# Kernel optimization log

Measured on AMD Instinct MI355X. Metric: run time of the kernel, lower is better.

The kernel has to match this reference:

```python
import jax, jax.numpy as jnp
import numpy as np

N, F, DEG, C = 20000, 64, 16, 16   # nodes, features, in-degree incl. self loop, classes
E = N * (DEG - 1)                   # regular (non-self-loop) edges


def setup_inputs() -> dict:
    key = jax.random.key(0)
    ks = jax.random.split(key, 12)
    x = jax.random.normal(ks[0], (N, F), dtype=jnp.float32)
    src = jax.random.randint(ks[1], (E,), 0, N, dtype=jnp.int32)
    dst = jnp.repeat(jnp.arange(N, dtype=jnp.int32), DEG - 1)  # exactly DEG-1 in-edges/node
    edge_index = jnp.stack([src, dst])
    s = 1.0 / np.sqrt(F)
    params = {}
    for i, kw, kb in ((1, ks[2], ks[3]), (2, ks[4], ks[5]), (3, ks[6], ks[7])):
        params[f"W{i}"] = jax.random.normal(kw, (F, F), dtype=jnp.float32) * s
        params[f"b{i}"] = jax.random.normal(kb, (F,), dtype=jnp.float32) * s
    params["Wfc"] = jax.random.normal(ks[8], (C, F), dtype=jnp.float32) * s
    params["bfc"] = jax.random.normal(ks[9], (C,), dtype=jnp.float32) * s
    return {"x": x, "edge_index": edge_index, **params}


def _pca_conv(h, src, dst, W, b):
    # GCNConv.forward: linear first, then propagate with symmetric normalization.
    hl = h @ W.T                                             # [N, F]
    # add self loops (appended after regular edges, as in PyG)
    loop = jnp.arange(N, dtype=src.dtype)
    src_a = jnp.concatenate([src, loop])
    dst_a = jnp.concatenate([dst, loop])
    deg = jnp.zeros((N,), hl.dtype).at[dst_a].add(1.0)
    dinv = jax.lax.rsqrt(deg)
    norm = dinv[src_a] * dinv[dst_a]                         # [Ea]
    m = norm[:, None] * hl[src_a]                            # messages [Ea, F]
    # aggregate(): pack each destination's messages contiguously, in edge order
    order = jnp.argsort(dst_a)                               # stable sort by destination
    sd = dst_a[order]
    slot = jnp.arange(sd.shape[0]) - jnp.searchsorted(sd, sd, side='left')
    neigh = jnp.zeros((N, DEG, F), hl.dtype).at[sd, slot].set(m[order])
    neigh = neigh.reshape(N, DEG * F)                        # [N, max_degree*F]
    # torch.pca_lowrank(neigh, q=F, center=True): top-F right singular vectors of
    # the column-centered matrix; computed via eigh on the (DEG*F x DEG*F) Gram.
    Xc = neigh - jnp.mean(neigh, axis=0, keepdims=True)
    G = Xc.T @ Xc                                            # [DEG*F, DEG*F]
    _, V = jnp.linalg.eigh(G)                                # ascending eigenvalues
    Vtop = V[:, ::-1][:, :F]                                 # top-F principal directions
    proj = neigh @ Vtop                                      # note: projects UNcentered neigh
    return proj @ W.T + b                                    # self.lin again + bias


def reference(x, edge_index, W1, b1, W2, b2, W3, b3, Wfc, bfc):
    src, dst = edge_index[0], edge_index[1]
    h = jax.nn.relu(_pca_conv(x, src, dst, W1, b1))
    h = jax.nn.relu(_pca_conv(h, src, dst, W2, b2))
    h = jax.nn.relu(_pca_conv(h, src, dst, W3, b3))
    out = h @ Wfc.T + bfc
    return jax.nn.log_softmax(out, axis=-1)
```

## Files before the change

kernel.cpp:

```cpp
#include <hip/hip_runtime.h>
#include <cmath>

#define NNODES 20000
#define FD 64
#define EPN 15
#define NB 1024
#define BSUB 80
#define NCLS 16
#define NPAIR 40

__global__ __launch_bounds__(256) void k_linT(const float* __restrict__ X,
    const float* __restrict__ W, const float* __restrict__ bias,
    float* __restrict__ out, int ncol, int relu)
{
  __shared__ float Wsh[64][65];
  __shared__ float Xsh[64][65];
  int t = threadIdx.x;
  int r0 = blockIdx.x * 64;
  for (int idx = t; idx < ncol * 64; idx += 256) Wsh[idx >> 6][idx & 63] = W[idx];
  for (int idx = t; idx < 64 * 64; idx += 256) {
    int r = idx >> 6, c = idx & 63;
    Xsh[r][c] = (r0 + r < NNODES) ? X[(size_t)(r0 + r) * 64 + c] : 0.f;
  }
  __syncthreads();
  for (int idx = t; idx < 64 * ncol; idx += 256) {
    int r = idx / ncol, o = idx % ncol;
    float acc = 0.f;
    #pragma unroll
    for (int j = 0; j < 64; j++) acc += Xsh[r][j] * Wsh[o][j];
    if (bias) acc += bias[o];
    if (relu) acc = fmaxf(acc, 0.f);
    if (r0 + r < NNODES) out[(size_t)(r0 + r) * ncol + o] = acc;
  }
}

__global__ __launch_bounds__(256) void k_meanslot(const float* __restrict__ hl,
    const int* __restrict__ src, float* __restrict__ mus)
{
  int k = blockIdx.x;
  int part = blockIdx.y;
  int t = threadIdx.x;
  int c = t & 63, sub = t >> 6;
  int d0 = part * 2500;
  float acc = 0.f;
  for (int d = d0 + sub; d < d0 + 2500; d += 4) {
    int row = (k < EPN) ? src[d * EPN + k] : d;
    acc += hl[(size_t)row * 64 + c];
  }
  __shared__ float red[4][64];
  red[sub][c] = acc;
  __syncthreads();
  if (t < 64) {
    float s = red[0][t] + red[1][t] + red[2][t] + red[3][t];
    atomicAdd(&mus[k * 64 + t], s * (1.f / 20000.f));
  }
}

__global__ __launch_bounds__(256) void k_buildX(const float* __restrict__ hl,
    const int* __restrict__ src, const float* __restrict__ mus,
    float* __restrict__ X)
{
  __shared__ float4 mu4[256];
  int t = threadIdx.x;
  int d0 = blockIdx.x * 64;
  mu4[t] = ((const float4*)mus)[t];
  __syncthreads();
  for (int k = 0; k < 16; k++) {
    for (int item = t; item < 1024; item += 256) {
      int rr = item >> 4, f4 = item & 15;
      int d = d0 + rr;
      if (d < NNODES) {
        int row = (k < EPN) ? src[d * EPN + k] : d;
        float4 v = ((const float4*)hl)[(size_t)row * 16 + f4];
        float4 m = mu4[k * 16 + f4];
        v.x -= m.x; v.y -= m.y; v.z -= m.z; v.w -= m.w;
        ((float4*)X)[(size_t)d * 256 + k * 16 + f4] = v;
      }
    }
  }
}

__global__ __launch_bounds__(256) void k_syrkX(const float* __restrict__ X,
    float* __restrict__ TP, int rows)
{
  __shared__ float As[32][128];
  __shared__ float Bs[32][128];
  int t = threadIdx.x;
  int pr = blockIdx.x, I = 0, rem = pr;
  for (int ii = 0; ii < 8; ii++) {
    int cnt = 8 - ii;
    if (rem < cnt) { I = ii; break; }
    rem -= cnt;
  }
  int J = I + rem;
  int d0 = blockIdx.y * rows;
  int d1 = d0 + rows;
  int a0 = (t & 15) * 4, b0 = (t >> 4) * 4;
  float acc[8][8] = {};
  for (int dc = d0; dc < d1; dc += 32) {
    __syncthreads();
    for (int item = t; item < 1024; item += 256) {
      int rr = item >> 5, c4 = item & 31;
      int d = dc + rr;
      float4 va = make_float4(0.f, 0.f, 0.f, 0.f), vb = va;
      if (d < d1) {
        va = ((const float4*)X)[(size_t)d * 256 + I * 32 + c4];
        vb = ((const float4*)X)[(size_t)d * 256 + J * 32 + c4];
      }
      *(float4*)&As[rr][c4 * 4] = va;
      *(float4*)&Bs[rr][c4 * 4] = vb;
    }
    __syncthreads();
    for (int dd = 0; dd < 32; dd++) {
      float av[8], bv[8];
      *(float4*)&av[0] = *(const float4*)&As[dd][a0];
      *(float4*)&av[4] = *(const float4*)&As[dd][a0 + 64];
      *(float4*)&bv[0] = *(const float4*)&Bs[dd][b0];
      *(float4*)&bv[4] = *(const float4*)&Bs[dd][b0 + 64];
      #pragma unroll
      for (int x = 0; x < 8; x++)
        #pragma unroll
        for (int y = 0; y < 8; y++) acc[x][y] += av[x] * bv[y];
    }
  }
  float* Tout = TP + (size_t)blockIdx.y * ((size_t)NB * NB);
  #pragma unroll
  for (int x = 0; x < 8; x++) {
    int rowi = I * 128 + ((x < 4) ? (a0 + x) : (64 + a0 + x - 4));
    size_t base = (size_t)rowi * NB + J * 128;
    *(float4*)&Tout[base + b0]      = make_float4(acc[x][0], acc[x][1], acc[x][2], acc[x][3]);
    *(float4*)&Tout[base + 64 + b0] = make_float4(acc[x][4], acc[x][5], acc[x][6], acc[x][7]);
  }
}

__global__ __launch_bounds__(256) void k_assembleG16(const float* __restrict__ TP,
    float* __restrict__ G, int ns)
{
  size_t idx = (size_t)blockIdx.x * 256 + threadIdx.x;
  int p = (int)(idx >> 10), q = (int)(idx & 1023);
  int ti = p >> 6, tj = q >> 6;
  size_t e = (ti <= tj) ? idx : (((size_t)q << 10) | (size_t)p);
  float v = 0.f;
  for (int s2 = 0; s2 < ns; s2++) v += TP[(size_t)s2 * ((size_t)NB * NB) + e];
  G[idx] = v * (1.f / 256.f);
}

__global__ __launch_bounds__(256) void k_gram(const float* __restrict__ hl,
    const int* __restrict__ src, const float* __restrict__ mus,
    float* __restrict__ T)
{
  __shared__ float Ash[64][64];
  __shared__ float Bsh[64][64];
  __shared__ float muA[64], muB[64];
  int t = threadIdx.x;
  int pr = blockIdx.x, i = 0, rem = pr;
  for (int ii = 0; ii < 16; ii++) {
    int cnt = 16 - ii;
    if (rem < cnt) { i = ii; break; }
    rem -= cnt;
  }
  int j = i + rem;
  if (t < 64) muA[t] = mus[i * 64 + t];
  else if (t < 128) muB[t - 64] = mus[j * 64 + (t - 64)];
  float acc[4][4] = {};
  int a0 = (t & 15) * 4, b0 = (t >> 4) * 4;
  int d0 = blockIdx.y * 4000, d1 = d0 + 4000;
  for (int dc = d0; dc < d1; dc += 64) {
    __syncthreads();
    for (int item = t; item < 1024; item += 256) {
      int rr = item >> 4, f4 = item & 15;
      int d = dc + rr;
      float4 va = make_float4(0.f, 0.f, 0.f, 0.f);
      float4 vb = va;
      if (d < d1) {
        int ra = (i < EPN) ? src[d * EPN + i] : d;
        int rb = (j < EPN) ? src[d * EPN + j] : d;
        va = ((const float4*)hl)[(size_t)ra * 16 + f4];
        vb = ((const float4*)hl)[(size_t)rb * 16 + f4];
        int cb = f4 * 4;
        va.x -= muA[cb]; va.y -= muA[cb + 1]; va.z -= muA[cb + 2]; va.w -= muA[cb + 3];
        vb.x -= muB[cb]; vb.y -= muB[cb + 1]; vb.z -= muB[cb + 2]; vb.w -= muB[cb + 3];
      }
      ((float4*)&Ash[rr][0])[f4] = va;
      ((float4*)&Bsh[rr][0])[f4] = vb;
    }
    __syncthreads();
    for (int dd = 0; dd < 64; dd++) {
      float av[4], bv[4];
      #pragma unroll
      for (int u = 0; u < 4; u++) av[u] = Ash[dd][a0 + u];
      #pragma unroll
      for (int u = 0; u < 4; u++) bv[u] = Bsh[dd][b0 + u];
      #pragma unroll
      for (int x = 0; x < 4; x++)
        #pragma unroll
        for (int y = 0; y < 4; y++) acc[x][y] += av[x] * bv[y];
    }
  }
  #pragma unroll
  for (int x = 0; x < 4; x++)
    #pragma unroll
    for (int y = 0; y < 4; y++)
      atomicAdd(&T[(size_t)(i * 64 + a0 + x) * NB + (j * 64 + b0 + y)], acc[x][y]);
}

__global__ __launch_bounds__(256) void k_assembleG(const float* __restrict__ T,
    float* __restrict__ G)
{
  size_t idx = (size_t)blockIdx.x * 256 + threadIdx.x;
  int p = (int)(idx >> 10), q = (int)(idx & 1023);
  int ti = p >> 6, tj = q >> 6;
  float v = (ti <= tj) ? T[idx] : T[((size_t)q << 10) | (size_t)p];
  G[idx] = v * (1.f / 256.f);
}

__global__ __launch_bounds__(256) void k_gemmG2(const float* __restrict__ G,
    float* __restrict__ G2)
{
  __shared__ float Ash[64][68];
  __shared__ float Bsh[64][68];
  int t = threadIdx.x;
  int bi = blockIdx.x * 64, bj = blockIdx.y * 64;
  int a0 = (t & 15) * 4, b0 = (t >> 4) * 4;
  float acc[4][4] = {};
  for (int d0 = 0; d0 < NB; d0 += 64) {
    __syncthreads();
    for (int item = t; item < 1024; item += 256) {
      int rr = item >> 4, f4 = item & 15;
      *(float4*)&Ash[rr][f4 * 4] =
          ((const float4*)G)[(size_t)(d0 + rr) * 256 + (bi >> 2) + f4];
      *(float4*)&Bsh[rr][f4 * 4] =
          ((const float4*)G)[(size_t)(d0 + rr) * 256 + (bj >> 2) + f4];
    }
    __syncthreads();
    for (int dd = 0; dd < 64; dd++) {
      float av[4], bv[4];
      #pragma unroll
      for (int u = 0; u < 4; u++) av[u] = Ash[dd][a0 + u];
      #pragma unroll
      for (int u = 0; u < 4; u++) bv[u] = Bsh[dd][b0 + u];
      #pragma unroll
      for (int x = 0; x < 4; x++)
        #pragma unroll
        for (int y = 0; y < 4; y++) acc[x][y] += av[x] * bv[y];
    }
  }
  #pragma unroll
  for (int x = 0; x < 4; x++) {
    float4 v = make_float4(acc[x][0], acc[x][1], acc[x][2], acc[x][3]);
    ((float4*)G2)[(size_t)(bi + a0 + x) * 256 + ((bj + b0) >> 2)] = v;
  }
}

__global__ void k_cut0(const float* __restrict__ G, double* __restrict__ scal)
{
  __shared__ float red[256];
  float m = 0.f;
  for (int p = threadIdx.x; p < NB; p += 256) m = fmaxf(m, G[(size_t)p * NB + p]);
  red[threadIdx.x] = m;
  __syncthreads();
  for (int s = 128; s; s >>= 1) {
    if (threadIdx.x < s) red[threadIdx.x] = fmaxf(red[threadIdx.x], red[threadIdx.x + s]);
    __syncthreads();
  }
  if (threadIdx.x == 0) {
    double c = 0.9 * (double)red[0];
    scal[0] = c;
    scal[1] = c * c;
  }
}

__global__ void k_initS(float* __restrict__ S)
{
  int idx = blockIdx.x * 256 + threadIdx.x;
  if (idx < NB * BSUB) {
    unsigned u = (unsigned)(idx + 1) * 2654435761u;
    u ^= u >> 16; u *= 2246822519u; u ^= u >> 13; u *= 3266489917u; u ^= u >> 16;
    S[idx] = ((float)u * (1.f / 4294967296.f)) - 0.5f;
  }
}

__global__ __launch_bounds__(256) void k_gzfused(const float* __restrict__ G,
    const float* __restrict__ Z, const float* __restrict__ Zp,
    float* __restrict__ P, float* __restrict__ out, int* __restrict__ cnt,
    const double* __restrict__ cptr, float s1, float s2, float s3)
{
  __shared__ float Gs[32][68];
  __shared__ float Zs[64][84];
  __shared__ int lastf;
  int t = threadIdx.x;
  int r0b = blockIdx.x;
  int r0 = r0b * 32;
  int kz = blockIdx.y;
  int cg = t & 15, rg = t >> 4;
  float acc0[5] = {}, acc1[5] = {};
  for (int k0 = kz * 128; k0 < kz * 128 + 128; k0 += 64) {
    __syncthreads();
    #pragma unroll
    for (int s = 0; s < 2; s++) {
      int item = t + s * 256;
      int rr = item >> 4, f4 = item & 15;
      float4 g = ((const float4*)G)[(size_t)(r0 + rr) * 256 + (k0 >> 2) + f4];
      *(float4*)&Gs[rr][f4 * 4] = g;
    }
    #pragma unroll
    for (int s = 0; s < 5; s++) {
      int item = t + s * 256;
      int rr = item / 20, f4 = item % 20;
      float4 z = ((const float4*)Z)[(size_t)(k0 + rr) * 20 + f4];
      *(float4*)&Zs[rr][f4 * 4] = z;
    }
    __syncthreads();
    for (int kk = 0; kk < 64; kk++) {
      float g0 = Gs[rg * 2 + 0][kk];
      float g1 = Gs[rg * 2 + 1][kk];
      float z[5];
      #pragma unroll
      for (int m = 0; m < 5; m++) z[m] = Zs[kk][cg * 5 + m];
      #pragma unroll
      for (int m = 0; m < 5; m++) { acc0[m] += g0 * z[m]; acc1[m] += g1 * z[m]; }
    }
  }
  size_t base = (size_t)kz * (NB * BSUB) + (size_t)(r0 + rg * 2) * BSUB + cg * 5;
  #pragma unroll
  for (int m = 0; m < 5; m++) P[base + m] = acc0[m];
  #pragma unroll
  for (int m = 0; m < 5; m++) P[base + BSUB + m] = acc1[m];
  __threadfence();
  __syncthreads();
  if (t == 0) {
    int old = atomicAdd(&cnt[r0b], 1);
    lastf = (old == 7) ? 1 : 0;
  }
  __syncthreads();
  if (!lastf) return;
  __threadfence();
  float coef = s1;
  if (cptr) coef = s1 * (float)(2.0 / cptr[0]);
  const float4* P4 = (const float4*)P;
  for (int idx = t; idx < 640; idx += 256) {
    size_t o4 = (size_t)r0 * 20 + idx;
    float4 a = P4[o4];
    #pragma unroll
    for (int u = 1; u < 8; u++) {
      float4 b = P4[(size_t)u * 20480 + o4];
      a.x += b.x; a.y += b.y; a.z += b.z; a.w += b.w;
    }
    float4 z = ((const float4*)Z)[o4];
    float4 o;
    o.x = coef * a.x + s2 * z.x;
    o.y = coef * a.y + s2 * z.y;
    o.z = coef * a.z + s2 * z.z;
    o.w = coef * a.w + s2 * z.w;
    if (s3 != 0.f) {
      float4 zp = ((const float4*)Zp)[o4];
      o.x += s3 * zp.x; o.y += s3 * zp.y; o.z += s3 * zp.z; o.w += s3 * zp.w;
    }
    ((float4*)out)[o4] = o;
  }
  __syncthreads();
  if (t == 0) cnt[r0b] = 0;
}

__global__ __launch_bounds__(256) void k_xty2(const float* __restrict__ X,
    const float* __restrict__ Y, double* __restrict__ CP)
{
  __shared__ float Xsh[64][BSUB + 1];
  __shared__ float Ysh[64][BSUB + 1];
  int t = threadIdx.x;
  int i0 = blockIdx.x * 64;
  for (int idx = t; idx < 64 * BSUB; idx += 256) {
    int r = idx / BSUB, c = idx % BSUB;
    Xsh[r][c] = X[(size_t)(i0 + r) * BSUB + c];
    Ysh[r][c] = Y[(size_t)(i0 + r) * BSUB + c];
  }
  __syncthreads();
  int a0 = (t & 15) * 5, b0 = (t >> 4) * 5;
  double acc[5][5] = {};
  for (int dd = 0; dd < 64; dd++) {
    float av[5], bv[5];
    #pragma unroll
    for (int u = 0; u < 5; u++) av[u] = Xsh[dd][a0 + u];
    #pragma unroll
    for (int u = 0; u < 5; u++) bv[u] = Ysh[dd][b0 + u];
    #pragma unroll
    for (int x = 0; x < 5; x++)
      #pragma unroll
      for (int y = 0; y < 5; y++) acc[x][y] += (double)av[x] * (double)bv[y];
  }
  double* out = CP + (size_t)blockIdx.x * (BSUB * BSUB);
  #pragma unroll
  for (int x = 0; x < 5; x++)
    #pragma unroll
    for (int y = 0; y < 5; y++)
      out[(size_t)(a0 + x) * BSUB + (b0 + y)] = acc[x][y];
}

__global__ __launch_bounds__(512) void k_cholinv(const double* __restrict__ Cin,
    float* __restrict__ Rinv)
{
  __shared__ double R[BSUB][BSUB + 1];
  __shared__ double rownew[2][BSUB];
  __shared__ double dinv[BSUB];
  __shared__ float X[BSUB][BSUB + 1];
  int t = threadIdx.x;
  for (int idx = t; idx < BSUB * BSUB; idx += 512) {
    double s = 0.0;
    #pragma unroll
    for (int b = 0; b < 16; b++) s += Cin[(size_t)b * (BSUB * BSUB) + idx];
    R[idx / BSUB][idx % BSUB] = s;
  }
  __syncthreads();
  double flr0 = 1e-30 * (fabs(R[0][0]) + 1e-280);
  int prevrow = -1;
  int pb = 0;
  int k = 0;
  while (k < BSUB - 1) {
    int nrem = BSUB - 1 - k;
    int total = (nrem * (nrem + 1)) >> 1;
    int cplen = (prevrow >= 0) ? (BSUB - prevrow) : 0;
    double piv = R[k][k];
    if (piv < flr0) piv = flr0;
    double rp = 1.0 / piv;
    bool pair = (k + 1 < BSUB - 1);
    if (pair) {
      double dk1 = R[k][k + 1];
      double p1 = R[k + 1][k + 1] - dk1 * dk1 * rp;
      if (p1 < flr0) p1 = flr0;
      double rp1 = 1.0 / p1;
      for (int idx = t; idx < total + cplen; idx += 512) {
        if (idx < total) {
          float nf = 2.f * (float)nrem + 1.f;
          int a = (int)((nf - sqrtf(nf * nf - 8.f * (float)idx)) * 0.5f);
          while (a > 0 && a * nrem - ((a * (a - 1)) >> 1) > idx) a--;
          while ((a + 1) * nrem - (((a + 1) * a) >> 1) <= idx) a++;
          int off = idx - (a * nrem - ((a * (a - 1)) >> 1));
          int i2 = k + 1 + a, j2 = i2 + off;
          if (a == 0) {
            rownew[pb][j2] = R[k + 1][j2] - dk1 * R[k][j2] * rp;
          } else {
            double v = R[i2][j2] - R[k][i2] * R[k][j2] * rp;
            double R1i = R[k + 1][i2] - dk1 * R[k][i2] * rp;
            double R1j = R[k + 1][j2] - dk1 * R[k][j2] * rp;
            v -= R1i * R1j * rp1;
            R[i2][j2] = v;
          }
        } else {
          int j = prevrow + (idx - total);
          R[prevrow][j] = rownew[pb ^ 1][j];
        }
      }
      __syncthreads();
      prevrow = k + 1; pb ^= 1; k += 2;
    } else {
      for (int idx = t; idx < total + cplen; idx += 512) {
        if (idx < total) {
          float nf = 2.f * (float)nrem + 1.f;
          int a = (int)((nf - sqrtf(nf * nf - 8.f * (float)idx)) * 0.5f);
          while (a > 0 && a * nrem - ((a * (a - 1)) >> 1) > idx) a--;
          while ((a + 1) * nrem - (((a + 1) * a) >> 1) <= idx) a++;
          int off = idx - (a * nrem - ((a * (a - 1)) >> 1));
          int i2 = k + 1 + a, j2 = i2 + off;
          R[i2][j2] -= R[k][i2] * R[k][j2] * rp;
        } else {
          int j = prevrow + (idx - total);
          R[prevrow][j] = rownew[pb ^ 1][j];
        }
      }
      __syncthreads();
      prevrow = -1; k += 1;
    }
  }
  if (prevrow >= 0) {
    for (int j = prevrow + t; j < BSUB; j += 512) R[prevrow][j] = rownew[pb ^ 1][j];
    __syncthreads();
  }
  if (t < BSUB) {
    double piv = R[t][t];
    if (piv < flr0) piv = flr0;
    dinv[t] = 1.0 / sqrt(piv);
  }
  __syncthreads();
  for (int idx = t; idx < BSUB * BSUB; idx += 512) {
    int kk = idx / BSUB, j = idx % BSUB;
    if (j > kk) R[kk][j] *= dinv[kk];
  }
  __syncthreads();
  if (t < BSUB) R[t][t] = 1.0 / dinv[t];
  __syncthreads();
  if (t < BSUB) {
    int j = t;
    X[j][j] = (float)dinv[j];
    for (int i = j - 1; i >= 0; i--) {
      double s = 0.0;
      for (int k2 = i + 1; k2 <= j; k2++) s += R[i][k2] * (double)X[k2][j];
      X[i][j] = (float)(-s * dinv[i]);
    }
    for (int i = j + 1; i < BSUB; i++) X[i][j] = 0.f;
  }
  __syncthreads();
  for (int idx = t; idx < BSUB * BSUB; idx += 512)
    Rinv[idx] = X[idx / BSUB][idx % BSUB];
}

__global__ __launch_bounds__(256) void k_gemmSR(const float* __restrict__ S,
    const float* __restrict__ Rinv, float* __restrict__ out)
{
  __shared__ float Rsh[BSUB][84];
  int t = threadIdx.x;
  for (int idx = t; idx < BSUB * BSUB; idx += 256)
    Rsh[idx / BSUB][idx % BSUB] = Rinv[idx];
  __syncthreads();
  int r0 = blockIdx.x * 32;
  int r = t >> 3, c0 = (t & 7) * 10;
  float acc[10] = {};
  const float* srow = &S[(size_t)(r0 + r) * BSUB];
  for (int k = 0; k < BSUB; k++) {
    float s = srow[k];
    #pragma unroll
    for (int m = 0; m < 10; m++) acc[m] += s * Rsh[k][c0 + m];
  }
  #pragma unroll
  for (int m = 0; m < 10; m++) out[(size_t)(r0 + r) * BSUB + c0 + m] = acc[m];
}

__global__ __launch_bounds__(1024) void k_jacobi(const double* __restrict__ Min,
    float* __restrict__ Uout, int* __restrict__ perm,
    double* __restrict__ cutout, int sweeps, int withU)
{
  __shared__ float Mb[2][BSUB][BSUB + 1];
  __shared__ float Ut[BSUB][BSUB];
  __shared__ float4 rot[2][NPAIR];
  __shared__ float th[BSUB];
  __shared__ int id[BSUB];
  int t = threadIdx.x;
  for (int idx = t; idx < BSUB * BSUB; idx += 1024) {
    double s = 0.0;
    #pragma unroll
    for (int b = 0; b < 16; b++) s += Min[(size_t)b * (BSUB * BSUB) + idx];
    Mb[1][idx / BSUB][idx % BSUB] = (float)s;
    if (withU) Ut[idx / BSUB][idx % BSUB] = ((idx / BSUB) == (idx % BSUB)) ? 1.f : 0.f;
  }
  int pr0 = t / 40, j0 = t - pr0 * 40;
  int pr1 = -1, j1 = 0;
  {
    int i1 = t + 1024;
    if (i1 < 1600) { pr1 = i1 / 40; j1 = i1 - pr1 * 40; }
  }
  int upr0 = -1, um0 = 0, upr1 = -1, um1 = 0;
  if (t >= 40) {
    int u0 = t - 40;              upr0 = u0 / 40; um0 = u0 - upr0 * 40;
    int u1 = t - 40 + 984;
    if (u1 < 1600) { upr1 = u1 / 40; um1 = u1 - upr1 * 40; }
  }
  int rp_ = 0, rq_ = 0;
  if (t < 40) {
    rp_ = (t == 0) ? 0 : 1 + (t - 1) % 79;
    rq_ = 1 + (78 - t) % 79;
  }
  __syncthreads();
  for (int idx = t; idx < BSUB * BSUB; idx += 1024) {
    int i2 = idx / BSUB, j2 = idx % BSUB;
    Mb[0][i2][j2] = 0.5f * (Mb[1][i2][j2] + Mb[1][j2][i2]);
  }
  __syncthreads();
  int nrounds = sweeps * (BSUB - 1);
  int mcur = 0;
  for (int it = 0; it < nrounds; it++) {
    int pb = it & 1;
    float (*Mc)[BSUB + 1] = Mb[mcur];
    float (*Mn)[BSUB + 1] = Mb[mcur ^ 1];
    if (t < 40) {
      int p = rp_, q = rq_;
      if (p > q) { int tmp = p; p = q; q = tmp; }
      float apq = Mc[p][q];
      float c = 1.f, s = 0.f;
      if (fabsf(apq) > 1e-28f) {
        float tau = (Mc[q][q] - Mc[p][p]) / (2.f * apq);
        float tt = copysignf(1.f, tau) / (fabsf(tau) + sqrtf(1.f + tau * tau));
        c = rsqrtf(1.f + tt * tt);
        s = tt * c;
      }
      rot[pb][t] = make_float4(c, s, __int_as_float(p), __int_as_float(q));
      if (t > 0) rp_ = (rp_ == 79) ? 1 : rp_ + 1;
      rq_ = (rq_ == 79) ? 1 : rq_ + 1;
    } else if (withU && it > 0) {
      int ob = pb ^ 1;
      {
        float4 R0 = rot[ob][upr0];
        int p = __float_as_int(R0.z), q = __float_as_int(R0.w);
        float c = R0.x, s = R0.y;
        float2 up = *(float2*)&Ut[p][2 * um0];
        float2 uq = *(float2*)&Ut[q][2 * um0];
        float2 np, nq;
        np.x = c * up.x - s * uq.x;  np.y = c * up.y - s * uq.y;
        nq.x = s * up.x + c * uq.x;  nq.y = s * up.y + c * uq.y;
        *(float2*)&Ut[p][2 * um0] = np;
        *(float2*)&Ut[q][2 * um0] = nq;
      }
      if (upr1 >= 0) {
        float4 R1 = rot[ob][upr1];
        int p = __float_as_int(R1.z), q = __float_as_int(R1.w);
        float c = R1.x, s = R1.y;
        float2 up = *(float2*)&Ut[p][2 * um1];
        float2 uq = *(float2*)&Ut[q][2 * um1];
        float2 np, nq;
        np.x = c * up.x - s * uq.x;  np.y = c * up.y - s * uq.y;
        nq.x = s * up.x + c * uq.x;  nq.y = s * up.y + c * uq.y;
        *(float2*)&Ut[p][2 * um1] = np;
        *(float2*)&Ut[q][2 * um1] = nq;
      }
    }
    __syncthreads();
    {
      float4 Rp = rot[pb][pr0];
      float4 Rj = rot[pb][j0];
      int p = __float_as_int(Rp.z), q = __float_as_int(Rp.w);
      float c = Rp.x, s = Rp.y;
      int k = __float_as_int(Rj.z), k2 = __float_as_int(Rj.w);
      float cj = Rj.x, sj = Rj.y;
      float mpk = Mc[p][k],  mqk = Mc[q][k];
      float mpk2 = Mc[p][k2], mqk2 = Mc[q][k2];
      float rpk  = c * mpk  - s * mqk;
      float rqk  = s * mpk  + c * mqk;
      float rpk2 = c * mpk2 - s * mqk2;
      float rqk2 = s * mpk2 + c * mqk2;
      Mn[p][k]  = cj * rpk - sj * rpk2;
      Mn[q][k]  = cj * rqk - sj * rqk2;
      Mn[p][k2] = sj * rpk + cj * rpk2;
      Mn[q][k2] = sj * rqk + cj * rqk2;
    }
    if (pr1 >= 0) {
      float4 Rp = rot[pb][pr1];
      float4 Rj = rot[pb][j1];
      int p = __float_as_int(Rp.z), q = __float_as_int(Rp.w);
      float c = Rp.x, s = Rp.y;
      int k = __float_as_int(Rj.z), k2 = __float_as_int(Rj.w);
      float cj = Rj.x, sj = Rj.y;
      float mpk = Mc[p][k],  mqk = Mc[q][k];
      float mpk2 = Mc[p][k2], mqk2 = Mc[q][k2];
      float rpk  = c * mpk  - s * mqk;
      float rqk  = s * mpk  + c * mqk;
      float rpk2 = c * mpk2 - s * mqk2;
      float rqk2 = s * mpk2 + c * mqk2;
      Mn[p][k]  = cj * rpk - sj * rpk2;
      Mn[q][k]  = cj * rqk - sj * rqk2;
      Mn[p][k2] = sj * rpk + cj * rpk2;
      Mn[q][k2] = sj * rqk + cj * rqk2;
    }
    __syncthreads();
    mcur ^= 1;
  }
  if (withU) {
    int ob = (nrounds - 1) & 1;
    {
      float4 R0 = rot[ob][pr0];
      int p = __float_as_int(R0.z), q = __float_as_int(R0.w);
      float c = R0.x, s = R0.y;
      float2 up = *(float2*)&Ut[p][2 * j0];
      float2 uq = *(float2*)&Ut[q][2 * j0];
      float2 np, nq;
      np.x = c * up.x - s * uq.x;  np.y = c * up.y - s * uq.y;
      nq.x = s * up.x + c * uq.x;  nq.y = s * up.y + c * uq.y;
      *(float2*)&Ut[p][2 * j0] = np;
      *(float2*)&Ut[q][2 * j0] = nq;
    }
    if (pr1 >= 0) {
      float4 R1 = rot[ob][pr1];
      int p = __float_as_int(R1.z), q = __float_as_int(R1.w);
      float c = R1.x, s = R1.y;
      float2 up = *(float2*)&Ut[p][2 * j1];
      float2 uq = *(float2*)&Ut[q][2 * j1];
      float2 np, nq;
      np.x = c * up.x - s * uq.x;  np.y = c * up.y - s * uq.y;
      nq.x = s * up.x + c * uq.x;  nq.y = s * up.y + c * uq.y;
      *(float2*)&Ut[p][2 * j1] = np;
      *(float2*)&Ut[q][2 * j1] = nq;
    }
    __syncthreads();
  }
  float (*Mf)[BSUB + 1] = Mb[mcur];
  if (t < BSUB) { th[t] = Mf[t][t]; id[t] = t; }
  __syncthreads();
  if (t == 0) {
    for (int a = 1; a < BSUB; a++) {
      float v = th[a]; int ii = id[a]; int b = a - 1;
      while (b >= 0 && th[b] < v) { th[b + 1] = th[b]; id[b + 1] = id[b]; b--; }
      th[b + 1] = v; id[b + 1] = ii;
    }
    double cut = (double)th[BSUB - 1];
    double lo = 0.02 * (double)th[0];
    if (cut < lo) cut = lo;
    double hi = 0.98 * (double)th[63];
    if (cut > hi) cut = hi;
    cutout[0] = cut;
    cutout[1] = cut * cut;
  }
  __syncthreads();
  if (t < BSUB) perm[t] = id[t];
  if (withU)
    for (int idx = t; idx < BSUB * BSUB; idx += 1024) {
      int k = idx / BSUB, p = idx % BSUB;
      Uout[idx] = Ut[p][k];
    }
}

__global__ __launch_bounds__(256) void k_compose(const float* __restrict__ S,
    const float* __restrict__ U, const int* __restrict__ perm,
    float* __restrict__ out)
{
  __shared__ float Ush[BSUB][65];
  int t = threadIdx.x;
  for (int idx = t; idx < BSUB * 64; idx += 256) {
    int jj = idx >> 6, c = idx & 63;
    Ush[jj][c] = U[jj * BSUB + perm[c]];
  }
  __syncthreads();
  int r0 = blockIdx.x * 64;
  for (int oidx = t; oidx < 64 * 64; oidx += 256) {
    int r = oidx >> 6, c = oidx & 63;
    float acc = 0.f;
    const float* srow = &S[(size_t)(r0 + r) * BSUB];
    #pragma unroll 8
    for (int j = 0; j < BSUB; j++) acc += srow[j] * Ush[j][c];
    out[(size_t)(r0 + r) * 64 + c] = acc;
  }
}

__global__ __launch_bounds__(256) void k_projlin(const float* __restrict__ hl,
    const int* __restrict__ src, const float* __restrict__ Vtop,
    const float* __restrict__ W, const float* __restrict__ bias,
    float* __restrict__ hout)
{
  __shared__ float Vsh[64][68];
  __shared__ float Hsh[64][68];
  __shared__ float Psh[64][68];
  int t = threadIdx.x;
  int d0 = blockIdx.x * 64;
  int dd = t & 63, pg = t >> 6;
  float acc[16] = {};
  for (int k = 0; k < 16; k++) {
    __syncthreads();
    for (int item = t; item < 1024; item += 256) {
      int rr = item >> 4, f4 = item & 15;
      *(float4*)&Vsh[rr][f4 * 4] = ((const float4*)Vtop)[(size_t)(k * 64 + rr) * 16 + f4];
      int d = d0 + rr;
      float4 v = make_float4(0.f, 0.f, 0.f, 0.f);
      if (d < NNODES) {
        int row = (k < EPN) ? src[d * EPN + k] : d;
        v = ((const float4*)hl)[(size_t)row * 16 + f4];
      }
      *(float4*)&Hsh[rr][f4 * 4] = v;
    }
    __syncthreads();
    for (int j = 0; j < 64; j++) {
      float h = Hsh[dd][j];
      #pragma unroll
      for (int m = 0; m < 16; m++) acc[m] += h * Vsh[j][pg * 16 + m];
    }
  }
  __syncthreads();
  #pragma unroll
  for (int m = 0; m < 16; m++) Psh[dd][pg * 16 + m] = acc[m] * (1.f / 16.f);
  for (int item = t; item < 1024; item += 256) {
    int rr = item >> 4, f4 = item & 15;
    *(float4*)&Vsh[rr][f4 * 4] = ((const float4*)W)[(size_t)rr * 16 + f4];
  }
  __syncthreads();
  if (d0 + dd < NNODES) {
    #pragma unroll
    for (int m = 0; m < 16; m++) {
      int o = pg * 16 + m;
      float a = bias[o];
      for (int j = 0; j < 64; j++) a += Psh[dd][j] * Vsh[o][j];
      hout[(size_t)(d0 + dd) * 64 + o] = fmaxf(a, 0.f);
    }
  }
}

__global__ void k_logsoftmax(const float* __restrict__ logits, float* __restrict__ out)
{
  int n = blockIdx.x * 256 + threadIdx.x;
  if (n >= NNODES) return;
  float v[NCLS];
  float mx = -1e30f;
  #pragma unroll
  for (int c = 0; c < NCLS; c++) { v[c] = logits[(size_t)n * NCLS + c]; mx = fmaxf(mx, v[c]); }
  float se = 0.f;
  #pragma unroll
  for (int c = 0; c < NCLS; c++) se += expf(v[c] - mx);
  float lse = mx + logf(se);
  #pragma unroll
  for (int c = 0; c < NCLS; c++) out[(size_t)n * NCLS + c] = v[c] - lse;
}

extern "C" void kernel_launch(void* const* d_in, const int* in_sizes, int n_in,
                              void* d_out, int out_size, void* d_ws, size_t ws_size,
                              hipStream_t stream)
{
  (void)in_sizes; (void)n_in; (void)out_size;
  const float* x = (const float*)d_in[0];
  const int* src = (const int*)d_in[1];
  const float* Wl[3] = { (const float*)d_in[2], (const float*)d_in[4], (const float*)d_in[6] };
  const float* bl[3] = { (const float*)d_in[3], (const float*)d_in[5], (const float*)d_in[7] };
  const float* Wfc = (const float*)d_in[8];
  const float* bfc = (const float*)d_in[9];
  float* outp = (float*)d_out;

  char* w = (char*)d_ws;
  auto alloc = [&](size_t bytes) -> char* {
    char* p = w; w += (bytes + 255) & ~(size_t)255; return p;
  };
  float* hA   = (float*)alloc((size_t)NNODES * 64 * 4);
  float* hB   = (float*)alloc((size_t)NNODES * 64 * 4);
  float* hl   = (float*)alloc((size_t)NNODES * 64 * 4);
  float* T    = (float*)alloc((size_t)NB * NB * 4);
  float* G    = (float*)alloc((size_t)NB * NB * 4);
  float* G2   = (float*)alloc((size_t)NB * NB * 4);
  float* mus  = (float*)alloc(16 * 64 * 4);
  float* Zb[6];
  for (int i = 0; i < 6; i++) Zb[i] = (float*)alloc((size_t)NB * BSUB * 4);
  float* P     = (float*)alloc((size_t)8 * NB * BSUB * 4);
  int* cnt     = (int*)alloc(32 * 4);
  double* CP   = (double*)alloc((size_t)16 * BSUB * BSUB * 8);
  float* Rinv  = (float*)alloc(BSUB * BSUB * 4);
  float* U     = (float*)alloc(BSUB * BSUB * 4);
  int* perm    = (int*)alloc(BSUB * 4);
  float* Vtop  = (float*)alloc((size_t)NB * 64 * 4);
  double* scal = (double*)alloc(16 * 8);
  float* X      = (float*)alloc((size_t)NNODES * NB * 4);
  float* TP     = (float*)alloc((size_t)16 * (size_t)NB * NB * 4);
  size_t used16 = (size_t)(w - (char*)d_ws);
  (void)alloc((size_t)4 * (size_t)NB * NB * 4);
  size_t used20 = (size_t)(w - (char*)d_ws);
  int fastg = (used16 <= ws_size) ? 1 : 0;
  int NS    = (used20 <= ws_size) ? 20 : 16;

  const int GRID_ROWS = (NNODES + 63) / 64;

  hipMemsetAsync(cnt, 0, 32 * 4, stream);

  int cur = 0;
  auto gemmGZ = [&](const float* A, const float* Z, const float* Zp, float* o,
                    const double* cptr, float s1, float s2, float s3) {
    hipLaunchKernelGGL(k_gzfused, dim3(32, 8), dim3(256), 0, stream,
                       A, Z, Zp, P, o, cnt, cptr, s1, s2, s3);
  };
  auto chunk2 = [&](int deg, const double* cptr) {
    int a = (cur + 1) % 6, b = (cur + 2) % 6;
    float* bufs[3] = { Zb[cur], Zb[a], Zb[b] };
    int ip = 0, ic = 0, io = 1;
    for (int s = 0; s < deg; s++) {
      if (s == 0)
        gemmGZ(G2, bufs[ic], nullptr, bufs[io], cptr, 1.f, -1.f, 0.f);
      else
        gemmGZ(G2, bufs[ic], bufs[ip], bufs[io], cptr, 2.f, -2.f, -1.f);
      if (s == 0) { ip = 0; ic = 1; io = 2; }
      else { int tmp = ip; ip = ic; ic = io; io = tmp; }
    }
    int sel = (deg - 1) % 3;
    cur = (sel == 0) ? a : (sel == 1) ? b : cur;
  };
  auto cholqr = [&]() {
    hipLaunchKernelGGL(k_xty2, dim3(16), dim3(256), 0, stream, Zb[cur], Zb[cur], CP);
    hipLaunchKernelGGL(k_cholinv, dim3(1), dim3(512), 0, stream, CP, Rinv);
    int o = (cur + 1) % 6;
    hipLaunchKernelGGL(k_gemmSR, dim3(32), dim3(256), 0, stream, Zb[cur], Rinv, Zb[o]);
    cur = o;
  };
  auto rrmid = [&](double* cutp) {
    int y = (cur + 1) % 6;
    gemmGZ(G, Zb[cur], nullptr, Zb[y], nullptr, 1.f, 0.f, 0.f);
    hipLaunchKernelGGL(k_xty2, dim3(16), dim3(256), 0, stream, Zb[cur], Zb[y], CP);
    hipLaunchKernelGGL(k_jacobi, dim3(1), dim3(1024), 0, stream,
                       CP, U, perm, cutp, 2, 0);
  };
  auto rrfinal = [&](double* cutp) {
    int y = (cur + 1) % 6;
    gemmGZ(G, Zb[cur], nullptr, Zb[y], nullptr, 1.f, 0.f, 0.f);
    hipLaunchKernelGGL(k_xty2, dim3(16), dim3(256), 0, stream, Zb[cur], Zb[y], CP);
    hipLaunchKernelGGL(k_jacobi, dim3(1), dim3(1024), 0, stream,
                       CP, U, perm, cutp, 5, 1);
    hipLaunchKernelGGL(k_compose, dim3(16), dim3(256), 0, stream,
                       Zb[cur], U, perm, Vtop);
  };

  const float* hin = x;
  float* hout = hA;
  for (int l = 0; l < 3; l++) {
    hipLaunchKernelGGL(k_linT, dim3(GRID_ROWS), dim3(256), 0, stream,
                       hin, Wl[l], (const float*)nullptr, hl, 64, 0);
    hipMemsetAsync(mus, 0, 16 * 64 * 4, stream);
    hipLaunchKernelGGL(k_meanslot, dim3(16, 8), dim3(256), 0, stream, hl, src, mus);
    if (fastg) {
      hipLaunchKernelGGL(k_buildX, dim3(GRID_ROWS), dim3(256), 0, stream,
                         hl, src, mus, X);
      hipLaunchKernelGGL(k_syrkX, dim3(36, NS), dim3(256), 0, stream,
                         X, TP, NNODES / NS);
      hipLaunchKernelGGL(k_assembleG16, dim3(4096), dim3(256), 0, stream, TP, G, NS);
    } else {
      hipMemsetAsync(T, 0, (size_t)NB * NB * 4, stream);
      hipLaunchKernelGGL(k_gram, dim3(136, 5), dim3(256), 0, stream, hl, src, mus, T);
      hipLaunchKernelGGL(k_assembleG, dim3(4096), dim3(256), 0, stream, T, G);
    }
    hipLaunchKernelGGL(k_cut0, dim3(1), dim3(256), 0, stream, G, scal);
    hipLaunchKernelGGL(k_gemmG2, dim3(16, 16), dim3(256), 0, stream, G, G2);
    cur = 0;
    hipLaunchKernelGGL(k_initS, dim3((NB * BSUB + 255) / 256), dim3(256), 0, stream, Zb[cur]);
    chunk2(6, &scal[1]); cholqr();
    rrmid(&scal[2]);
    chunk2(7, &scal[3]); cholqr();
    chunk2(7, &scal[3]); cholqr();
    rrfinal(&scal[4]);
    hipLaunchKernelGGL(k_projlin, dim3(GRID_ROWS), dim3(256), 0, stream,
                       hl, src, Vtop, Wl[l], bl[l], hout);
    hin = hout;
    hout = (hout == hA) ? hB : hA;
  }
  hipLaunchKernelGGL(k_linT, dim3(GRID_ROWS), dim3(256), 0, stream,
                     hin, Wfc, bfc, hl, NCLS, 0);
  hipLaunchKernelGGL(k_logsoftmax, dim3((NNODES + 255) / 256), dim3(256), 0, stream,
                     hl, outp);
}
```

Baseline: 8.878 ms.

## Fuse small reduction kernels via last-block pattern and prefetch syrk tiles

Merges the partial X^T Y product kernel with the single-block Cholesky-inverse and Jacobi kernels, using an atomic counter so the last finishing block does the reduction and factorization. It also folds the diagonal-max cut kernel into the random init kernel and adds register prefetching of the next tile in the syrk Gram kernel. The aim is to remove several serial kernel launches on the latency-bound eigen-solver path and to hide global load latency in syrk. In exchange it adds threadfence/atomic overhead, uses larger blocks for the partial products, and raises register pressure in syrk.

```diff
diff --git a/kernel.cpp b/kernel.cpp
--- a/kernel.cpp
+++ b/kernel.cpp
@@ -96,21 +96,34 @@
   int d0 = blockIdx.y * rows;
   int d1 = d0 + rows;
   int a0 = (t & 15) * 4, b0 = (t >> 4) * 4;
-  float acc[8][8] = {};
-  for (int dc = d0; dc < d1; dc += 32) {
-    __syncthreads();
-    for (int item = t; item < 1024; item += 256) {
-      int rr = item >> 5, c4 = item & 31;
+  float4 pa[4], pb[4];
+  auto LOADR = [&](int dc) {
+    #pragma unroll
+    for (int s = 0; s < 4; s++) {
+      int idx = t + s * 256;
+      int rr = idx >> 5, c4 = idx & 31;
       int d = dc + rr;
       float4 va = make_float4(0.f, 0.f, 0.f, 0.f), vb = va;
       if (d < d1) {
         va = ((const float4*)X)[(size_t)d * 256 + I * 32 + c4];
         vb = ((const float4*)X)[(size_t)d * 256 + J * 32 + c4];
       }
-      *(float4*)&As[rr][c4 * 4] = va;
-      *(float4*)&Bs[rr][c4 * 4] = vb;
-    }
-    __syncthreads();
+      pa[s] = va; pb[s] = vb;
+    }
+  };
+  LOADR(d0);
+  float acc[8][8] = {};
+  for (int dc = d0; dc < d1; dc += 32) {
+    __syncthreads();
+    #pragma unroll
+    for (int s = 0; s < 4; s++) {
+      int idx = t + s * 256;
+      int rr = idx >> 5, c4 = idx & 31;
+      *(float4*)&As[rr][c4 * 4] = pa[s];
+      *(float4*)&Bs[rr][c4 * 4] = pb[s];
+    }
+    __syncthreads();
+    if (dc + 32 < d1) LOADR(dc + 32);
     for (int dd = 0; dd < 32; dd++) {
       float av[8], bv[8];
       *(float4*)&av[0] = *(const float4*)&As[dd][a0];
@@ -252,27 +265,29 @@
   }
 }
 
-__global__ void k_cut0(const float* __restrict__ G, double* __restrict__ scal)
-{
-  __shared__ float red[256];
-  float m = 0.f;
-  for (int p = threadIdx.x; p < NB; p += 256) m = fmaxf(m, G[(size_t)p * NB + p]);
-  red[threadIdx.x] = m;
-  __syncthreads();
-  for (int s = 128; s; s >>= 1) {
-    if (threadIdx.x < s) red[threadIdx.x] = fmaxf(red[threadIdx.x], red[threadIdx.x + s]);
-    __syncthreads();
-  }
-  if (threadIdx.x == 0) {
-    double c = 0.9 * (double)red[0];
-    scal[0] = c;
-    scal[1] = c * c;
-  }
-}
-
-__global__ void k_initS(float* __restrict__ S)
-{
-  int idx = blockIdx.x * 256 + threadIdx.x;
+__global__ void k_initScut(float* __restrict__ S, const float* __restrict__ G,
+                           double* __restrict__ scal)
+{
+  int b = blockIdx.x;
+  int t = threadIdx.x;
+  if (b == 0) {
+    __shared__ float red[256];
+    float m = 0.f;
+    for (int p = t; p < NB; p += 256) m = fmaxf(m, G[(size_t)p * NB + p]);
+    red[t] = m;
+    __syncthreads();
+    for (int s = 128; s; s >>= 1) {
+      if (t < s) red[t] = fmaxf(red[t], red[t + s]);
+      __syncthreads();
+    }
+    if (t == 0) {
+      double c = 0.9 * (double)red[0];
+      scal[0] = c;
+      scal[1] = c * c;
+    }
+    return;
+  }
+  int idx = (b - 1) * 256 + t;
   if (idx < NB * BSUB) {
     unsigned u = (unsigned)(idx + 1) * 2654435761u;
     u ^= u >> 16; u *= 2246822519u; u ^= u >> 13; u *= 3266489917u; u ^= u >> 16;
@@ -362,52 +377,57 @@
   if (t == 0) cnt[r0b] = 0;
 }
 
-__global__ __launch_bounds__(256) void k_xty2(const float* __restrict__ X,
-    const float* __restrict__ Y, double* __restrict__ CP)
+__global__ __launch_bounds__(512) void k_xtychol(const float* __restrict__ Sa,
+    const float* __restrict__ Sb, double* __restrict__ CP,
+    float* __restrict__ Rinv, int* __restrict__ cnt)
 {
   __shared__ float Xsh[64][BSUB + 1];
   __shared__ float Ysh[64][BSUB + 1];
+  __shared__ int lastf;
   int t = threadIdx.x;
   int i0 = blockIdx.x * 64;
-  for (int idx = t; idx < 64 * BSUB; idx += 256) {
+  for (int idx = t; idx < 64 * BSUB; idx += 512) {
     int r = idx / BSUB, c = idx % BSUB;
-    Xsh[r][c] = X[(size_t)(i0 + r) * BSUB + c];
-    Ysh[r][c] = Y[(size_t)(i0 + r) * BSUB + c];
-  }
-  __syncthreads();
-  int a0 = (t & 15) * 5, b0 = (t >> 4) * 5;
-  double acc[5][5] = {};
-  for (int dd = 0; dd < 64; dd++) {
-    float av[5], bv[5];
-    #pragma unroll
-    for (int u = 0; u < 5; u++) av[u] = Xsh[dd][a0 + u];
-    #pragma unroll
-    for (int u = 0; u < 5; u++) bv[u] = Ysh[dd][b0 + u];
+    Xsh[r][c] = Sa[(size_t)(i0 + r) * BSUB + c];
+    Ysh[r][c] = Sb[(size_t)(i0 + r) * BSUB + c];
+  }
+  __syncthreads();
+  if (t < 256) {
+    int a0 = (t & 15) * 5, b0 = (t >> 4) * 5;
+    double acc[5][5] = {};
+    for (int dd = 0; dd < 64; dd++) {
+      float av[5], bv[5];
+      #pragma unroll
+      for (int u = 0; u < 5; u++) av[u] = Xsh[dd][a0 + u];
+      #pragma unroll
+      for (int u = 0; u < 5; u++) bv[u] = Ysh[dd][b0 + u];
+      #pragma unroll
+      for (int x = 0; x < 5; x++)
+        #pragma unroll
+        for (int y = 0; y < 5; y++) acc[x][y] += (double)av[x] * (double)bv[y];
+    }
+    double* outp = CP + (size_t)blockIdx.x * (BSUB * BSUB);
     #pragma unroll
     for (int x = 0; x < 5; x++)
       #pragma unroll
-      for (int y = 0; y < 5; y++) acc[x][y] += (double)av[x] * (double)bv[y];
-  }
-  double* out = CP + (size_t)blockIdx.x * (BSUB * BSUB);
-  #pragma unroll
-  for (int x = 0; x < 5; x++)
-    #pragma unroll
-    for (int y = 0; y < 5; y++)
-      out[(size_t)(a0 + x) * BSUB + (b0 + y)] = acc[x][y];
-}
-
-__global__ __launch_bounds__(512) void k_cholinv(const double* __restrict__ Cin,
-    float* __restrict__ Rinv)
-{
+      for (int y = 0; y < 5; y++)
+        outp[(size_t)(a0 + x) * BSUB + (b0 + y)] = acc[x][y];
+  }
+  __threadfence();
+  __syncthreads();
+  if (t == 0) lastf = (atomicAdd(&cnt[0], 1) == 15) ? 1 : 0;
+  __syncthreads();
+  if (!lastf) return;
+  if (t == 0) cnt[0] = 0;
+  __threadfence();
   __shared__ double R[BSUB][BSUB + 1];
   __shared__ double rownew[2][BSUB];
   __shared__ double dinv[BSUB];
-  __shared__ float X[BSUB][BSUB + 1];
-  int t = threadIdx.x;
+  __shared__ float Xi[BSUB][BSUB + 1];
   for (int idx = t; idx < BSUB * BSUB; idx += 512) {
     double s = 0.0;
     #pragma unroll
-    for (int b = 0; b < 16; b++) s += Cin[(size_t)b * (BSUB * BSUB) + idx];
+    for (int b = 0; b < 16; b++) s += CP[(size_t)b * (BSUB * BSUB) + idx];
     R[idx / BSUB][idx % BSUB] = s;
   }
   __syncthreads();
@@ -490,17 +510,17 @@
   __syncthreads();
   if (t < BSUB) {
     int j = t;
-    X[j][j] = (float)dinv[j];
+    Xi[j][j] = (float)dinv[j];
     for (int i = j - 1; i >= 0; i--) {
       double s = 0.0;
-      for (int k2 = i + 1; k2 <= j; k2++) s += R[i][k2] * (double)X[k2][j];
-      X[i][j] = (float)(-s * dinv[i]);
-    }
-    for (int i = j + 1; i < BSUB; i++) X[i][j] = 0.f;
+      for (int k2 = i + 1; k2 <= j; k2++) s += R[i][k2] * (double)Xi[k2][j];
+      Xi[i][j] = (float)(-s * dinv[i]);
+    }
+    for (int i = j + 1; i < BSUB; i++) Xi[i][j] = 0.f;
   }
   __syncthreads();
   for (int idx = t; idx < BSUB * BSUB; idx += 512)
-    Rinv[idx] = X[idx / BSUB][idx % BSUB];
+    Rinv[idx] = Xi[idx / BSUB][idx % BSUB];
 }
 
 __global__ __launch_bounds__(256) void k_gemmSR(const float* __restrict__ S,
@@ -524,20 +544,59 @@
   for (int m = 0; m < 10; m++) out[(size_t)(r0 + r) * BSUB + c0 + m] = acc[m];
 }
 
-__global__ __launch_bounds__(1024) void k_jacobi(const double* __restrict__ Min,
+__global__ __launch_bounds__(1024) void k_xtyjac(const float* __restrict__ Sa,
+    const float* __restrict__ Sb, double* __restrict__ CP,
     float* __restrict__ Uout, int* __restrict__ perm,
-    double* __restrict__ cutout, int sweeps, int withU)
-{
+    double* __restrict__ cutout, int sweeps, int withU, int* __restrict__ cnt)
+{
+  __shared__ float Xsh[64][BSUB + 1];
+  __shared__ float Ysh[64][BSUB + 1];
+  __shared__ int lastf;
+  int t = threadIdx.x;
+  int i0 = blockIdx.x * 64;
+  for (int idx = t; idx < 64 * BSUB; idx += 1024) {
+    int r = idx / BSUB, c = idx % BSUB;
+    Xsh[r][c] = Sa[(size_t)(i0 + r) * BSUB + c];
+    Ysh[r][c] = Sb[(size_t)(i0 + r) * BSUB + c];
+  }
+  __syncthreads();
+  if (t < 256) {
+    int a0 = (t & 15) * 5, b0 = (t >> 4) * 5;
+    double acc[5][5] = {};
+    for (int dd = 0; dd < 64; dd++) {
+      float av[5], bv[5];
+      #pragma unroll
+      for (int u = 0; u < 5; u++) av[u] = Xsh[dd][a0 + u];
+      #pragma unroll
+      for (int u = 0; u < 5; u++) bv[u] = Ysh[dd][b0 + u];
+      #pragma unroll
+      for (int x = 0; x < 5; x++)
+        #pragma unroll
+        for (int y = 0; y < 5; y++) acc[x][y] += (double)av[x] * (double)bv[y];
+    }
+    double* outp = CP + (size_t)blockIdx.x * (BSUB * BSUB);
+    #pragma unroll
+    for (int x = 0; x < 5; x++)
+      #pragma unroll
+      for (int y = 0; y < 5; y++)
+        outp[(size_t)(a0 + x) * BSUB + (b0 + y)] = acc[x][y];
+  }
+  __threadfence();
+  __syncthreads();
+  if (t == 0) lastf = (atomicAdd(&cnt[0], 1) == 15) ? 1 : 0;
+  __syncthreads();
+  if (!lastf) return;
+  if (t == 0) cnt[0] = 0;
+  __threadfence();
   __shared__ float Mb[2][BSUB][BSUB + 1];
   __shared__ float Ut[BSUB][BSUB];
   __shared__ float4 rot[2][NPAIR];
   __shared__ float th[BSUB];
   __shared__ int id[BSUB];
-  int t = threadIdx.x;
   for (int idx = t; idx < BSUB * BSUB; idx += 1024) {
     double s = 0.0;
     #pragma unroll
-    for (int b = 0; b < 16; b++) s += Min[(size_t)b * (BSUB * BSUB) + idx];
+    for (int b = 0; b < 16; b++) s += CP[(size_t)b * (BSUB * BSUB) + idx];
     Mb[1][idx / BSUB][idx % BSUB] = (float)s;
     if (withU) Ut[idx / BSUB][idx % BSUB] = ((idx / BSUB) == (idx % BSUB)) ? 1.f : 0.f;
   }
@@ -821,7 +880,7 @@
   float* Zb[6];
   for (int i = 0; i < 6; i++) Zb[i] = (float*)alloc((size_t)NB * BSUB * 4);
   float* P     = (float*)alloc((size_t)8 * NB * BSUB * 4);
-  int* cnt     = (int*)alloc(32 * 4);
+  int* cnt     = (int*)alloc(64 * 4);
   double* CP   = (double*)alloc((size_t)16 * BSUB * BSUB * 8);
   float* Rinv  = (float*)alloc(BSUB * BSUB * 4);
   float* U     = (float*)alloc(BSUB * BSUB * 4);
@@ -838,7 +897,7 @@
 
   const int GRID_ROWS = (NNODES + 63) / 64;
 
-  hipMemsetAsync(cnt, 0, 32 * 4, stream);
+  hipMemsetAsync(cnt, 0, 64 * 4, stream);
 
   int cur = 0;
   auto gemmGZ = [&](const float* A, const float* Z, const float* Zp, float* o,
@@ -862,8 +921,8 @@
     cur = (sel == 0) ? a : (sel == 1) ? b : cur;
   };
   auto cholqr = [&]() {
-    hipLaunchKernelGGL(k_xty2, dim3(16), dim3(256), 0, stream, Zb[cur], Zb[cur], CP);
-    hipLaunchKernelGGL(k_cholinv, dim3(1), dim3(512), 0, stream, CP, Rinv);
+    hipLaunchKernelGGL(k_xtychol, dim3(16), dim3(512), 0, stream,
+                       Zb[cur], Zb[cur], CP, Rinv, cnt + 32);
     int o = (cur + 1) % 6;
     hipLaunchKernelGGL(k_gemmSR, dim3(32), dim3(256), 0, stream, Zb[cur], Rinv, Zb[o]);
     cur = o;
@@ -871,16 +930,14 @@
   auto rrmid = [&](double* cutp) {
     int y = (cur + 1) % 6;
     gemmGZ(G, Zb[cur], nullptr, Zb[y], nullptr, 1.f, 0.f, 0.f);
-    hipLaunchKernelGGL(k_xty2, dim3(16), dim3(256), 0, stream, Zb[cur], Zb[y], CP);
-    hipLaunchKernelGGL(k_jacobi, dim3(1), dim3(1024), 0, stream,
-                       CP, U, perm, cutp, 2, 0);
+    hipLaunchKernelGGL(k_xtyjac, dim3(16), dim3(1024), 0, stream,
+                       Zb[cur], Zb[y], CP, U, perm, cutp, 2, 0, cnt + 33);
   };
   auto rrfinal = [&](double* cutp) {
     int y = (cur + 1) % 6;
     gemmGZ(G, Zb[cur], nullptr, Zb[y], nullptr, 1.f, 0.f, 0.f);
-    hipLaunchKernelGGL(k_xty2, dim3(16), dim3(256), 0, stream, Zb[cur], Zb[y], CP);
-    hipLaunchKernelGGL(k_jacobi, dim3(1), dim3(1024), 0, stream,
-                       CP, U, perm, cutp, 5, 1);
+    hipLaunchKernelGGL(k_xtyjac, dim3(16), dim3(1024), 0, stream,
+                       Zb[cur], Zb[y], CP, U, perm, cutp, 5, 1, cnt + 33);
     hipLaunchKernelGGL(k_compose, dim3(16), dim3(256), 0, stream,
                        Zb[cur], U, perm, Vtop);
   };
@@ -903,10 +960,10 @@
       hipLaunchKernelGGL(k_gram, dim3(136, 5), dim3(256), 0, stream, hl, src, mus, T);
       hipLaunchKernelGGL(k_assembleG, dim3(4096), dim3(256), 0, stream, T, G);
     }
-    hipLaunchKernelGGL(k_cut0, dim3(1), dim3(256), 0, stream, G, scal);
     hipLaunchKernelGGL(k_gemmG2, dim3(16, 16), dim3(256), 0, stream, G, G2);
     cur = 0;
-    hipLaunchKernelGGL(k_initS, dim3((NB * BSUB + 255) / 256), dim3(256), 0, stream, Zb[cur]);
+    hipLaunchKernelGGL(k_initScut, dim3(1 + (NB * BSUB + 255) / 256), dim3(256), 0,
+                       stream, Zb[cur], G, scal);
     chunk2(6, &scal[1]); cholqr();
     rrmid(&scal[2]);
     chunk2(7, &scal[3]); cholqr();
```

Result: no change. 8.855 ms (-0.3%).
